# Performance work log

Hardware: AMD Instinct MI355X
Metric: run time of the kernel (lower is better)

The kernel has to match this reference:

```python
import jax, jax.numpy as jnp
import numpy as np

B, A, IN, H, NA = 256, 32, 512, 512, 64


def setup_inputs() -> dict:
    key = jax.random.key(0)
    ks = jax.random.split(key, 9)
    s = 1.0 / np.sqrt(H).astype(np.float32)
    si = 1.0 / np.sqrt(IN).astype(np.float32)
    return {
        "inputs": jax.random.normal(ks[0], (B * A, IN), jnp.float32),
        "hidden_state": jnp.zeros((B, A, H), jnp.float32),
        "W1": jax.random.normal(ks[1], (A, H, IN), jnp.float32) * si,
        "b1": jax.random.normal(ks[2], (A, H), jnp.float32) * si,
        "W_ih": jax.random.normal(ks[3], (A, 3 * H, H), jnp.float32) * s,
        "b_ih": jax.random.normal(ks[4], (A, 3 * H), jnp.float32) * s,
        "W_hh": jax.random.normal(ks[5], (A, 3 * H, H), jnp.float32) * s,
        "b_hh": jax.random.normal(ks[6], (A, 3 * H), jnp.float32) * s,
        "W2": jax.random.normal(ks[7], (A, NA, H), jnp.float32) * s,
        "b2": jax.random.normal(ks[8], (A, NA), jnp.float32) * s,
    }


def reference(inputs, hidden_state, W1, b1, W_ih, b_ih, W_hh, b_hh, W2, b2):
    # inputs: [B*A, IN] -> [B, A, IN]; per-agent distinct weights stacked on axis 0 (a)
    x = inputs.reshape(-1, A, IN)
    h_in = hidden_state  # [B, A, H]
    # fc1 + relu, grouped over agents
    x1 = jax.nn.relu(jnp.einsum('bai,ahi->bah', x, W1) + b1)
    # GRUCell (PyTorch gate layout: r, z, n)
    gx = jnp.einsum('bah,agh->bag', x1, W_ih) + b_ih   # [B, A, 3H]
    gh = jnp.einsum('bah,agh->bag', h_in, W_hh) + b_hh  # [B, A, 3H]
    gx_r, gx_z, gx_n = jnp.split(gx, 3, axis=-1)
    gh_r, gh_z, gh_n = jnp.split(gh, 3, axis=-1)
    r = jax.nn.sigmoid(gx_r + gh_r)
    z = jax.nn.sigmoid(gx_z + gh_z)
    n = jnp.tanh(gx_n + r * gh_n)
    h = (1.0 - z) * n + z * h_in  # [B, A, H]
    # fc2 per agent
    q = jnp.einsum('bah,anh->ban', h, W2) + b2  # [B, A, NA]
    # torch: cat(qs, dim=-1).view(-1, n_actions) == reshape to [B*A, NA]
    return q.reshape(-1, NA), h
```

## Files before the change

kernel.cpp:

```cpp
#include <hip/hip_runtime.h>
#include <hip/hip_bf16.h>


typedef __attribute__((ext_vector_type(8))) __bf16 bf16x8;
typedef __attribute__((ext_vector_type(4))) float  f32x4;

constexpr int NAGENT = 32;
constexpr int KC     = 512;

__device__ __forceinline__ bf16x8 cvt8(const float* p) {
  f32x4 u = *(const f32x4*)p;
  f32x4 v = *(const f32x4*)(p + 4);
  bf16x8 w;
  w[0] = (__bf16)u[0]; w[1] = (__bf16)u[1]; w[2] = (__bf16)u[2]; w[3] = (__bf16)u[3];
  w[4] = (__bf16)v[0]; w[5] = (__bf16)v[1]; w[6] = (__bf16)v[2]; w[7] = (__bf16)v[3];
  return w;
}
__device__ __forceinline__ float sigmoid_f(float x) { return 1.f / (1.f + __expf(-x)); }
__device__ __forceinline__ float tanh_f(float x) {
  float xc = fminf(fmaxf(x, -15.f), 15.f);
  float a = __expf(2.f * xc);
  return (a - 1.f) / (a + 1.f);
}
__device__ __forceinline__ int xcd_swz(int bid, int nwg) {
  return (bid & 7) * (nwg >> 3) + (bid >> 3);
}


__global__ __launch_bounds__(256) void prep_k(
    const float* __restrict__ hidden, __bf16* __restrict__ AF) {
  const int idx = blockIdx.x * 256 + threadIdx.x;
  const int kc = idx & 63;
  const int row = idx >> 6;
  const int a = row & 31, b = row >> 5;
  bf16x8 v = cvt8(hidden + (size_t)row * KC + kc * 8);
  *(bf16x8*)(AF + ((size_t)(a * 128 + 64 + kc) * 256 + b) * 8) = v;
}

__global__ __launch_bounds__(512, 2) void fc1_k(
    const float* __restrict__ inputs, const float* __restrict__ W1,
    const float* __restrict__ b1, __bf16* __restrict__ AF) {
  const int wg = xcd_swz(blockIdx.x, gridDim.x);
  const int a  = wg >> 3;
  const int n0 = (wg & 7) * 64;

  __shared__ __attribute__((aligned(16))) __bf16 lA[2][256][8][8];
  __shared__ __attribute__((aligned(16))) __bf16 lB[2][64][8][8];

  const int tid = threadIdx.x;
  const int lane = tid & 63;
  const int wave = tid >> 6;
  const int wm = wave >> 1, wn = wave & 1;
  const int lr = lane & 15, lk = lane >> 4;

  int arow[4], aks[4]; size_t aoff[4];
#pragma unroll
  for (int c = 0; c < 4; ++c) {
    const int idx = c * 512 + tid;
    arow[c] = idx >> 3; aks[c] = idx & 7;
    aoff[c] = ((size_t)arow[c] * NAGENT + a) * KC + aks[c] * 8;
  }
  const int brow = tid >> 3, bks = tid & 7;
  const size_t boff = ((size_t)a * 512 + n0 + brow) * KC + bks * 8;

  bf16x8 sA[4], sB;
  auto loadT = [&](int t) {
    const int kb = t * 64;
#pragma unroll
    for (int c = 0; c < 4; ++c) sA[c] = cvt8(inputs + aoff[c] + kb);
    sB = cvt8(W1 + boff + kb);
  };
  auto writeT = [&](int buf) {
#pragma unroll
    for (int c = 0; c < 4; ++c)
      *(bf16x8*)(&lA[buf][arow[c]][aks[c] ^ (arow[c] & 7)][0]) = sA[c];
    *(bf16x8*)(&lB[buf][brow][bks ^ (brow & 7)][0]) = sB;
  };

  f32x4 acc[4][2] = {};
  auto computeT = [&](int buf) {
#pragma unroll
    for (int s = 0; s < 2; ++s) {
      const int ks = s * 4 + lk;
      bf16x8 af[4];
#pragma unroll
      for (int i = 0; i < 4; ++i) {
        const int row = wm * 64 + i * 16 + lr;
        af[i] = *(const bf16x8*)(&lA[buf][row][ks ^ (row & 7)][0]);
      }
#pragma unroll
      for (int cb = 0; cb < 2; ++cb) {
        const int br = wn * 32 + cb * 16 + lr;
        bf16x8 bv = *(const bf16x8*)(&lB[buf][br][ks ^ (br & 7)][0]);
#pragma unroll
        for (int i = 0; i < 4; ++i)
          acc[i][cb] = __builtin_amdgcn_mfma_f32_16x16x32_bf16(af[i], bv, acc[i][cb], 0, 0, 0);
      }
    }
  };

  loadT(0); writeT(0);
  int cur = 0;
#pragma unroll 1
  for (int t = 0; t < 8; ++t) {
    __syncthreads();
    if (t < 7) loadT(t + 1);
    computeT(cur);
    if (t < 7) { writeT(cur ^ 1); cur ^= 1; }
  }

#pragma unroll
  for (int cb = 0; cb < 2; ++cb) {
    const int col = n0 + wn * 32 + cb * 16 + lr;
    const int kc = col >> 3, c7 = col & 7;
    const float bias = b1[(size_t)a * 512 + col];
#pragma unroll
    for (int i = 0; i < 4; ++i) {
      const int r0 = wm * 64 + i * 16 + lk * 4;
#pragma unroll
      for (int e = 0; e < 4; ++e) {
        const float v = fmaxf(acc[i][cb][e] + bias, 0.f);
        AF[((size_t)(a * 128 + kc) * 256 + r0 + e) * 8 + c7] = (__bf16)v;
      }
    }
  }
}

__global__ __launch_bounds__(512, 4) void gru_k(
    const __bf16* __restrict__ AF,
    const float* __restrict__ Wih, const float* __restrict__ bih,
    const float* __restrict__ Whh, const float* __restrict__ bhh,
    float* __restrict__ hout, __bf16* __restrict__ hbf) {
  const int wg = xcd_swz(blockIdx.x, gridDim.x);
  const int a  = wg >> 4;
  const int n0 = (wg & 15) * 32;

  __shared__ __attribute__((aligned(16))) __bf16 lB[2][96][8][8];

  const int tid = threadIdx.x;
  const int lane = tid & 63;
  const int wm = tid >> 6;
  const int lr = lane & 15, lk = lane >> 4;

  const int br0 = tid >> 3, bks = tid & 7;
  const int br1 = 64 + (tid >> 3);
  auto wrow = [&](int r) {
    return (size_t)a * 1536 + (r >> 5) * 512 + n0 + (r & 31);
  };
  const size_t boff0 = wrow(br0) * KC + bks * 8;
  const size_t boff1 = (tid < 256 ? wrow(br1) * KC + bks * 8 : 0);

  size_t aBase[2];
#pragma unroll
  for (int i = 0; i < 2; ++i)
    aBase[i] = (size_t)a * 262144 + (size_t)lk * 2048 +
               (size_t)(wm * 32 + i * 16 + lr) * 8;

  bf16x8 sB0, sB1;
  auto loadB = [&](int t) {
    const float* W = (t < 8) ? Wih : Whh;
    const int kb = (t & 7) * 64;
    sB0 = cvt8(W + boff0 + kb);
    if (tid < 256) sB1 = cvt8(W + boff1 + kb);
  };
  auto writeB = [&](int buf) {
    *(bf16x8*)(&lB[buf][br0][bks ^ (br0 & 7)][0]) = sB0;
    if (tid < 256) *(bf16x8*)(&lB[buf][br1][bks ^ (br1 & 7)][0]) = sB1;
  };

  bf16x8 af0[2][2], af1[2][2];
  auto loadA = [&](bf16x8 (&dst)[2][2], int t) {
#pragma unroll
    for (int s = 0; s < 2; ++s)
#pragma unroll
      for (int i = 0; i < 2; ++i)
        dst[s][i] = *(const bf16x8*)(AF + aBase[i] + (size_t)t * 16384 + s * 8192);
  };

  f32x4 accR[2][2] = {}, accZ[2][2] = {}, accXN[2][2] = {}, accHN[2][2] = {};
  auto compute = [&](int buf, bf16x8 (&af)[2][2], f32x4 (&accN)[2][2]) {
#pragma unroll
    for (int s = 0; s < 2; ++s) {
      const int ks = s * 4 + lk;
#pragma unroll
      for (int cc = 0; cc < 2; ++cc) {
        const int rr = cc * 16 + lr;
        const int sw = ks ^ (rr & 7);
        bf16x8 bR = *(const bf16x8*)(&lB[buf][rr][sw][0]);
        bf16x8 bZ = *(const bf16x8*)(&lB[buf][32 + rr][sw][0]);
        bf16x8 bN = *(const bf16x8*)(&lB[buf][64 + rr][sw][0]);
#pragma unroll
        for (int i = 0; i < 2; ++i) {
          accR[i][cc] = __builtin_amdgcn_mfma_f32_16x16x32_bf16(af[s][i], bR, accR[i][cc], 0, 0, 0);
          accZ[i][cc] = __builtin_amdgcn_mfma_f32_16x16x32_bf16(af[s][i], bZ, accZ[i][cc], 0, 0, 0);
          accN[i][cc] = __builtin_amdgcn_mfma_f32_16x16x32_bf16(af[s][i], bN, accN[i][cc], 0, 0, 0);
        }
      }
    }
  };

  loadB(0); writeB(0);
  loadA(af0, 0);
#pragma unroll
  for (int t = 0; t < 8; ++t) {
    __syncthreads();
    loadB(t + 1);
    if (t & 1) { loadA(af0, t + 1); compute(1, af1, accXN); }
    else       { loadA(af1, t + 1); compute(0, af0, accXN); }
    writeB((t & 1) ^ 1);
  }
#pragma unroll
  for (int t = 8; t < 16; ++t) {
    __syncthreads();
    if (t < 15) loadB(t + 1);
    if (t & 1) { if (t < 15) loadA(af0, t + 1); compute(1, af1, accHN); }
    else       { if (t < 15) loadA(af1, t + 1); compute(0, af0, accHN); }
    if (t < 15) writeB((t & 1) ^ 1);
  }

#pragma unroll
  for (int cc = 0; cc < 2; ++cc) {
    const int col = n0 + cc * 16 + lr;
    const size_t ab = (size_t)a * 1536 + col;
    const float br_ = bih[ab] + bhh[ab];
    const float bz_ = bih[ab + 512] + bhh[ab + 512];
    const float bxn = bih[ab + 1024];
    const float bhn = bhh[ab + 1024];
    const size_t hfb = ((size_t)(a * 128 + 64 + (col >> 3)) * 256) * 8 + (col & 7);
#pragma unroll
    for (int i = 0; i < 2; ++i) {
      const int r0 = wm * 32 + i * 16 + lk * 4;
#pragma unroll
      for (int e = 0; e < 4; ++e) {
        const float hprev = (float)AF[hfb + (size_t)(r0 + e) * 8];
        const float r = sigmoid_f(accR[i][cc][e] + br_);
        const float z = sigmoid_f(accZ[i][cc][e] + bz_);
        const float n = tanh_f((accXN[i][cc][e] + bxn) + r * (accHN[i][cc][e] + bhn));
        const float h = (1.f - z) * n + z * hprev;
        const size_t o = ((size_t)(r0 + e) * NAGENT + a) * KC + col;
        hout[o] = h;
        hbf[o] = (__bf16)h;
      }
    }
  }
}

template <bool ABF16, int ACT, bool OBF16>
__global__ __launch_bounds__(256) void gemm64(
    const void* __restrict__ Ap, const float* __restrict__ Wp,
    const float* __restrict__ bp, void* __restrict__ Op, const int N) {
  constexpr int BM = 64, MT = 4;
  const int NT = N >> 6;
  const int wg = xcd_swz(blockIdx.x, gridDim.x);
  const int a  = wg / (MT * NT);
  const int rem = wg % (MT * NT);
  const int n0 = (rem / MT) * 64;
  const int b0 = (rem % MT) * BM;

  __shared__ __attribute__((aligned(16))) __bf16 lA[2][4][64][8];
  __shared__ __attribute__((aligned(16))) __bf16 lB[2][4][64][8];

  const int tid = threadIdx.x;
  const int lane = tid & 63;
  const int wn = tid >> 6;
  const int lr = lane & 15, lk = lane >> 4;

  const int ar = tid >> 2, aks = tid & 3;
  const size_t aoff = ((size_t)(b0 + ar) * NAGENT + a) * KC + aks * 8;
  const size_t boff = ((size_t)a * N + n0 + ar) * KC + aks * 8;

  const float*  Af = (const float*)Ap;
  const __bf16* Ab = (const __bf16*)Ap;

  bf16x8 sA, sB;
  auto loadT = [&](int t) {
    if constexpr (ABF16) sA = *(const bf16x8*)(Ab + aoff + t * 32);
    else                 sA = cvt8(Af + aoff + t * 32);
    sB = cvt8(Wp + boff + t * 32);
  };
  auto writeT = [&](int buf) {
    *(bf16x8*)(&lA[buf][aks][ar][0]) = sA;
    *(bf16x8*)(&lB[buf][aks][ar][0]) = sB;
  };

  f32x4 acc[4] = {};
  auto computeT = [&](int buf) {
    bf16x8 bv = *(const bf16x8*)(&lB[buf][lk][wn * 16 + lr][0]);
#pragma unroll
    for (int i = 0; i < 4; ++i) {
      bf16x8 af = *(const bf16x8*)(&lA[buf][lk][i * 16 + lr][0]);
      acc[i] = __builtin_amdgcn_mfma_f32_16x16x32_bf16(af, bv, acc[i], 0, 0, 0);
    }
  };

  loadT(0); writeT(0);
  int cur = 0;
#pragma unroll 1
  for (int t = 0; t < KC / 32; ++t) {
    __syncthreads();
    if (t + 1 < KC / 32) loadT(t + 1);
    computeT(cur);
    if (t + 1 < KC / 32) { writeT(cur ^ 1); cur ^= 1; }
  }

  const int col = n0 + wn * 16 + lr;
  const float bias = bp[(size_t)a * N + col];
#pragma unroll
  for (int i = 0; i < 4; ++i) {
    const int r0 = b0 + i * 16 + lk * 4;
#pragma unroll
    for (int e = 0; e < 4; ++e) {
      float v = acc[i][e] + bias;
      if (ACT == 1) v = fmaxf(v, 0.f);
      const size_t o = ((size_t)(r0 + e) * NAGENT + a) * N + col;
      if constexpr (OBF16) ((__bf16*)Op)[o] = (__bf16)v;
      else                 ((float*)Op)[o]  = v;
    }
  }
}

extern "C" void kernel_launch(void* const* d_in, const int* in_sizes, int n_in,
                              void* d_out, int out_size, void* d_ws, size_t ws_size,
                              hipStream_t stream) {
  const float* inputs = (const float*)d_in[0];
  const float* hidden = (const float*)d_in[1];
  const float* W1   = (const float*)d_in[2];
  const float* b1   = (const float*)d_in[3];
  const float* W_ih = (const float*)d_in[4];
  const float* b_ih = (const float*)d_in[5];
  const float* W_hh = (const float*)d_in[6];
  const float* b_hh = (const float*)d_in[7];
  const float* W2   = (const float*)d_in[8];
  const float* b2   = (const float*)d_in[9];

  float* out_q = (float*)d_out;
  float* out_h = out_q + (size_t)8192 * 64;

  char* ws = (char*)d_ws;
  __bf16* AF  = (__bf16*)(ws);
  __bf16* hbf = (__bf16*)(ws + ((size_t)16 << 20));

  prep_k<<<2048, 256, 0, stream>>>(hidden, AF);
  fc1_k<<<256, 512, 0, stream>>>(inputs, W1, b1, AF);
  gru_k<<<512, 512, 0, stream>>>(AF, W_ih, b_ih, W_hh, b_hh, out_h, hbf);
  gemm64<true, 0, false><<<128, 256, 0, stream>>>(hbf, W2, b2, out_q, 64);
}
```

Before: 115.0 us.

## Widen GRU tile to 64 columns with 1024-thread blocks and 2x8 wave grid

The GRU gate kernel now processes 64 output columns per block instead of 32, with 16 waves arranged as 8 row-waves by 2 column-waves and 1024 threads per block, halving the grid to 256 blocks. Each A fragment loaded from global memory is reused across more weight columns per block, cutting redundant activation reads. The A-operand register double-buffering is removed and the K loops are no longer unrolled, which lowers register pressure but exposes global load latency inside compute. With only 256 blocks of 1024 threads, occupancy and latency hiding depend on fitting multiple blocks per CU.

Result: faster. 112.7 us (-2.0%).

```diff
diff --git a/kernel.cpp b/kernel.cpp
--- a/kernel.cpp
+++ b/kernel.cpp
@@ -126,29 +126,31 @@
   }
 }
 
-__global__ __launch_bounds__(512, 4) void gru_k(
+__global__ __launch_bounds__(1024, 4) void gru_k(
     const __bf16* __restrict__ AF,
     const float* __restrict__ Wih, const float* __restrict__ bih,
     const float* __restrict__ Whh, const float* __restrict__ bhh,
     float* __restrict__ hout, __bf16* __restrict__ hbf) {
   const int wg = xcd_swz(blockIdx.x, gridDim.x);
-  const int a  = wg >> 4;
-  const int n0 = (wg & 15) * 32;
-
-  __shared__ __attribute__((aligned(16))) __bf16 lB[2][96][8][8];
+  const int a  = wg >> 3;
+  const int n0 = (wg & 7) * 64;
+
+  __shared__ __attribute__((aligned(16))) __bf16 lB[2][192][8][8];
 
   const int tid = threadIdx.x;
   const int lane = tid & 63;
-  const int wm = tid >> 6;
+  const int wave = tid >> 6;
+  const int wm = wave >> 1;
+  const int wc = wave & 1;
   const int lr = lane & 15, lk = lane >> 4;
 
   const int br0 = tid >> 3, bks = tid & 7;
-  const int br1 = 64 + (tid >> 3);
+  const int br1 = 128 + (tid >> 3);
   auto wrow = [&](int r) {
-    return (size_t)a * 1536 + (r >> 5) * 512 + n0 + (r & 31);
+    return (size_t)a * 1536 + (r >> 6) * 512 + n0 + (r & 63);
   };
   const size_t boff0 = wrow(br0) * KC + bks * 8;
-  const size_t boff1 = (tid < 256 ? wrow(br1) * KC + bks * 8 : 0);
+  const size_t boff1 = (tid < 512 ? wrow(br1) * KC + bks * 8 : 0);
 
   size_t aBase[2];
 #pragma unroll
@@ -161,34 +163,31 @@
     const float* W = (t < 8) ? Wih : Whh;
     const int kb = (t & 7) * 64;
     sB0 = cvt8(W + boff0 + kb);
-    if (tid < 256) sB1 = cvt8(W + boff1 + kb);
+    if (tid < 512) sB1 = cvt8(W + boff1 + kb);
   };
   auto writeB = [&](int buf) {
     *(bf16x8*)(&lB[buf][br0][bks ^ (br0 & 7)][0]) = sB0;
-    if (tid < 256) *(bf16x8*)(&lB[buf][br1][bks ^ (br1 & 7)][0]) = sB1;
-  };
-
-  bf16x8 af0[2][2], af1[2][2];
-  auto loadA = [&](bf16x8 (&dst)[2][2], int t) {
+    if (tid < 512) *(bf16x8*)(&lB[buf][br1][bks ^ (br1 & 7)][0]) = sB1;
+  };
+
+  f32x4 accR[2][2] = {}, accZ[2][2] = {}, accXN[2][2] = {}, accHN[2][2] = {};
+  auto compute = [&](int buf, int t, f32x4 (&accN)[2][2]) {
+    bf16x8 af[2][2];
 #pragma unroll
     for (int s = 0; s < 2; ++s)
 #pragma unroll
       for (int i = 0; i < 2; ++i)
-        dst[s][i] = *(const bf16x8*)(AF + aBase[i] + (size_t)t * 16384 + s * 8192);
-  };
-
-  f32x4 accR[2][2] = {}, accZ[2][2] = {}, accXN[2][2] = {}, accHN[2][2] = {};
-  auto compute = [&](int buf, bf16x8 (&af)[2][2], f32x4 (&accN)[2][2]) {
+        af[s][i] = *(const bf16x8*)(AF + aBase[i] + (size_t)t * 16384 + s * 8192);
 #pragma unroll
     for (int s = 0; s < 2; ++s) {
       const int ks = s * 4 + lk;
 #pragma unroll
       for (int cc = 0; cc < 2; ++cc) {
-        const int rr = cc * 16 + lr;
+        const int rr = wc * 32 + cc * 16 + lr;
         const int sw = ks ^ (rr & 7);
         bf16x8 bR = *(const bf16x8*)(&lB[buf][rr][sw][0]);
-        bf16x8 bZ = *(const bf16x8*)(&lB[buf][32 + rr][sw][0]);
-        bf16x8 bN = *(const bf16x8*)(&lB[buf][64 + rr][sw][0]);
+        bf16x8 bZ = *(const bf16x8*)(&lB[buf][64 + rr][sw][0]);
+        bf16x8 bN = *(const bf16x8*)(&lB[buf][128 + rr][sw][0]);
 #pragma unroll
         for (int i = 0; i < 2; ++i) {
           accR[i][cc] = __builtin_amdgcn_mfma_f32_16x16x32_bf16(af[s][i], bR, accR[i][cc], 0, 0, 0);
@@ -200,27 +199,25 @@
   };
 
   loadB(0); writeB(0);
-  loadA(af0, 0);
-#pragma unroll
+  int cur = 0;
+#pragma unroll 1
   for (int t = 0; t < 8; ++t) {
     __syncthreads();
     loadB(t + 1);
-    if (t & 1) { loadA(af0, t + 1); compute(1, af1, accXN); }
-    else       { loadA(af1, t + 1); compute(0, af0, accXN); }
-    writeB((t & 1) ^ 1);
-  }
-#pragma unroll
+    compute(cur, t, accXN);
+    writeB(cur ^ 1); cur ^= 1;
+  }
+#pragma unroll 1
   for (int t = 8; t < 16; ++t) {
     __syncthreads();
     if (t < 15) loadB(t + 1);
-    if (t & 1) { if (t < 15) loadA(af0, t + 1); compute(1, af1, accHN); }
-    else       { if (t < 15) loadA(af1, t + 1); compute(0, af0, accHN); }
-    if (t < 15) writeB((t & 1) ^ 1);
+    compute(cur, t, accHN);
+    if (t < 15) { writeB(cur ^ 1); cur ^= 1; }
   }
 
 #pragma unroll
   for (int cc = 0; cc < 2; ++cc) {
-    const int col = n0 + cc * 16 + lr;
+    const int col = n0 + wc * 32 + cc * 16 + lr;
     const size_t ab = (size_t)a * 1536 + col;
     const float br_ = bih[ab] + bhh[ab];
     const float bz_ = bih[ab + 512] + bhh[ab + 512];
@@ -342,6 +339,6 @@
 
   prep_k<<<2048, 256, 0, stream>>>(hidden, AF);
   fc1_k<<<256, 512, 0, stream>>>(inputs, W1, b1, AF);
-  gru_k<<<512, 512, 0, stream>>>(AF, W_ih, b_ih, W_hh, b_hh, out_h, hbf);
+  gru_k<<<256, 1024, 0, stream>>>(AF, W_ih, b_ih, W_hh, b_hh, out_h, hbf);
   gemm64<true, 0, false><<<128, 256, 0, stream>>>(hbf, W2, b2, out_q, 64);
 }
```
